# Kernel tuning notes

Measured on AMD Instinct MI355X. Metric: run time of the kernel, lower is better.

## Reference

```python
import jax, jax.numpy as jnp
import numpy as np
import math

DIM = 768
FFN_DIM = 4 * DIM
EPS = 1e-5

def layer_norm(x, gamma, beta):
    mu = jnp.mean(x, axis=-1, keepdims=True)
    var = jnp.var(x, axis=-1, keepdims=True)
    return (x - mu) * jax.lax.rsqrt(var + EPS) * gamma + beta

def setup_inputs() -> dict:
    key = jax.random.key(0)
    ks = jax.random.split(key, 8)
    b, n, d = 8, 2048, DIM
    s = 1.0 / math.sqrt(d)
    x = jax.random.normal(ks[0], (b, n, d), dtype=jnp.float32)
    Wq = jax.random.normal(ks[1], (d, d), dtype=jnp.float32) * s
    Wk = jax.random.normal(ks[2], (d, d), dtype=jnp.float32) * s
    Wv = jax.random.normal(ks[3], (d, d), dtype=jnp.float32) * s
    W1 = jax.random.normal(ks[4], (d, FFN_DIM), dtype=jnp.float32) * s
    b1 = jnp.zeros((FFN_DIM,), dtype=jnp.float32)
    W2 = jax.random.normal(ks[5], (FFN_DIM, d), dtype=jnp.float32) * (1.0 / math.sqrt(FFN_DIM))
    b2 = jnp.zeros((d,), dtype=jnp.float32)
    g1 = jnp.ones((d,), dtype=jnp.float32); be1 = jnp.zeros((d,), dtype=jnp.float32)
    g2 = jnp.ones((d,), dtype=jnp.float32); be2 = jnp.zeros((d,), dtype=jnp.float32)
    return {"x": x, "Wq": Wq, "Wk": Wk, "Wv": Wv, "ln1_g": g1, "ln1_b": be1,
            "W1": W1, "b1": b1, "W2": W2, "b2": b2, "ln2_g": g2, "ln2_b": be2}

def reference(x, Wq, Wk, Wv, ln1_g, ln1_b, W1, b1, W2, b2, ln2_g, ln2_b):
    # Self-attention (single head, full dim; dropout in eval mode => identity)
    Q = jnp.einsum('bnd,de->bne', x, Wq)
    K = jnp.einsum('bnd,de->bne', x, Wk)
    V = jnp.einsum('bnd,de->bne', x, Wv)
    scores = jnp.einsum('bnd,bmd->bnm', Q, K) / math.sqrt(DIM)  # [b,n,n]
    attn = jax.nn.softmax(scores, axis=-1)
    O = jnp.einsum('bnm,bmd->bnd', attn, V)
    h = layer_norm(x + O, ln1_g, ln1_b)
    # FFN with exact GELU (torch nn.GELU default)
    hidden = jax.nn.gelu(jnp.einsum('bnd,df->bnf', h, W1) + b1, approximate=False)
    out = jnp.einsum('bnf,fd->bnd', hidden, W2) + b2
    return layer_norm(h + out, ln2_g, ln2_b)
```

## Files before the change

### kernel.cpp

```cpp
#include <hip/hip_runtime.h>
#include <hip/hip_bf16.h>
#include <math.h>

using u16 = unsigned short;
typedef __bf16 bf16x8 __attribute__((ext_vector_type(8)));
typedef float f32x4 __attribute__((ext_vector_type(4)));
typedef u16 u16x8 __attribute__((ext_vector_type(8)));

__device__ __forceinline__ u16 f2b(float f) {
  union { float f; unsigned u; } c; c.f = f;
  unsigned r = c.u + 0x7fffu + ((c.u >> 16) & 1u);
  return (u16)(r >> 16);
}
__device__ __forceinline__ float b2f(u16 h) {
  union { unsigned u; float f; } c; c.u = ((unsigned)h) << 16;
  return c.f;
}

__device__ __forceinline__ float fast_gelu(float t) {
  float y = fminf(1.5957691216f * t + 0.07135481283f * t * t * t, 80.f);
  float e = __expf(y);
  return t * e * (1.0f / (e + 1.0f));
}

#define EPI_BF16 0
#define EPI_BF16_SCALE 1
#define EPI_GELU_BIAS 2
#define EPI_F32_BIAS 3

#define GLDS16(src, dst)                                                     \
  __builtin_amdgcn_global_load_lds(                                          \
      (const __attribute__((address_space(1))) void*)(src),                  \
      (__attribute__((address_space(3))) void*)(dst), 16, 0, 0)

__device__ __forceinline__ int xswz(int o, int n) {
  int q = n >> 3, r = n & 7, x = o & 7, i = o >> 3;
  return (x < r ? x * (q + 1) : r * (q + 1) + (x - r) * q) + i;
}

template <int EPI>
__device__ __forceinline__ void epi_store(
    void* Cg, const float* bias, float v, long long off, int ccol, float scale)
{
  if (EPI == EPI_BF16) {
    ((u16*)Cg)[off] = f2b(v);
  } else if (EPI == EPI_BF16_SCALE) {
    ((u16*)Cg)[off] = f2b(v * scale);
  } else if (EPI == EPI_GELU_BIAS) {
    ((u16*)Cg)[off] = f2b(fast_gelu(v + bias[ccol]));
  } else {
    ((float*)Cg)[off] = v + bias[ccol];
  }
}

template <int EPI>
__global__ __launch_bounds__(512, 2) void gemm256(
    const u16* __restrict__ Ag, const u16* __restrict__ Bg,
    void* __restrict__ Cg, const float* __restrict__ bias,
    int nbx, int K, float scale, int lda, int ldb, int ldc,
    long long sAz, long long sBz, long long sCz)
{
  __shared__ __align__(16) u16 lds[65536];

  const int tid = threadIdx.x;
  const int wave = tid >> 6, lane = tid & 63;
  const int wr = wave >> 2, wc = wave & 3;
  const int id = xswz(blockIdx.x, gridDim.x);
  const int bx = id % nbx, by = id / nbx;
  const int m0 = by * 256, n0 = bx * 256;
  const long long z = blockIdx.z;
  const u16* A = Ag + z * sAz + (long long)m0 * lda;
  const u16* B = Bg + z * sBz + (long long)n0 * ldb;

  const int rA = wave * 32 + (lane >> 2);
  const int slot = (lane & 3) ^ ((rA >> 1) & 3);
  const u16* a0 = A + (long long)rA * lda + slot * 8;
  const u16* a1 = a0 + (long long)16 * lda;
  const u16* b0 = B + (long long)rA * ldb + slot * 8;
  const u16* b1 = b0 + (long long)16 * ldb;
  const int d0 = wave * 32 * 32;
  const int d1 = (wave * 32 + 16) * 32;

  int offA[8], offB[4];
#pragma unroll
  for (int mf = 0; mf < 8; ++mf) {
    int r = wr * 128 + mf * 16 + (lane & 15);
    int b = r * 64 + ((lane >> 4) << 4);
    offA[mf] = b ^ (((b >> 7) & 3) << 4);
  }
#pragma unroll
  for (int nf = 0; nf < 4; ++nf) {
    int r = wc * 64 + nf * 16 + (lane & 15);
    int b = r * 64 + ((lane >> 4) << 4);
    offB[nf] = b ^ (((b >> 7) & 3) << 4);
  }

  f32x4 acc[8][4];
#pragma unroll
  for (int m = 0; m < 8; ++m)
#pragma unroll
    for (int n = 0; n < 4; ++n) acc[m][n] = f32x4{0.f, 0.f, 0.f, 0.f};

  const char* ldsc = (const char*)lds;
  const int NT = K >> 6;

  GLDS16(a0, lds + 0 * 8192 + d0);  GLDS16(a1, lds + 0 * 8192 + d1);
  GLDS16(b0, lds + 2 * 8192 + d0);  GLDS16(b1, lds + 2 * 8192 + d1);
  GLDS16(a0 + 32, lds + 1 * 8192 + d0);  GLDS16(a1 + 32, lds + 1 * 8192 + d1);
  GLDS16(b0 + 32, lds + 3 * 8192 + d0);  GLDS16(b1 + 32, lds + 3 * 8192 + d1);
  asm volatile("s_waitcnt vmcnt(4)" ::: "memory");
  asm volatile("s_barrier" ::: "memory");

  for (int t = 0; t < NT; ++t) {
    const int buf = t & 1, nb = buf ^ 1;
    const int kc = (t + 1 < NT) ? ((t + 1) << 6) : 0;
    const char* pA0 = ldsc + (buf * 4 + 0) * 16384;
    const char* pA1 = ldsc + (buf * 4 + 1) * 16384;
    const char* pB0 = ldsc + (buf * 4 + 2) * 16384;
    const char* pB1 = ldsc + (buf * 4 + 3) * 16384;
    u16* q = lds + nb * 4 * 8192;

    bf16x8 Af[4], Bf[4];

    GLDS16(a0 + kc, q + 0 * 8192 + d0);
    GLDS16(a1 + kc, q + 0 * 8192 + d1);
#pragma unroll
    for (int m = 0; m < 4; ++m) Af[m] = *(const bf16x8*)(pA0 + offA[m]);
#pragma unroll
    for (int n = 0; n < 4; ++n) Bf[n] = *(const bf16x8*)(pB0 + offB[n]);
    asm volatile("s_barrier" ::: "memory");
    __builtin_amdgcn_s_setprio(1);
#pragma unroll
    for (int m = 0; m < 4; ++m)
#pragma unroll
      for (int n = 0; n < 4; ++n)
        acc[m][n] = __builtin_amdgcn_mfma_f32_16x16x32_bf16(Af[m], Bf[n], acc[m][n], 0, 0, 0);
    __builtin_amdgcn_s_setprio(0);
    asm volatile("s_barrier" ::: "memory");

    GLDS16(b0 + kc, q + 2 * 8192 + d0);
    GLDS16(b1 + kc, q + 2 * 8192 + d1);
#pragma unroll
    for (int m = 0; m < 4; ++m) Af[m] = *(const bf16x8*)(pA0 + offA[4 + m]);
    asm volatile("s_barrier" ::: "memory");
    __builtin_amdgcn_s_setprio(1);
#pragma unroll
    for (int m = 0; m < 4; ++m)
#pragma unroll
      for (int n = 0; n < 4; ++n)
        acc[4 + m][n] = __builtin_amdgcn_mfma_f32_16x16x32_bf16(Af[m], Bf[n], acc[4 + m][n], 0, 0, 0);
    __builtin_amdgcn_s_setprio(0);
    asm volatile("s_waitcnt vmcnt(4)" ::: "memory");
    asm volatile("s_barrier" ::: "memory");

    GLDS16(a0 + kc + 32, q + 1 * 8192 + d0);
    GLDS16(a1 + kc + 32, q + 1 * 8192 + d1);
#pragma unroll
    for (int m = 0; m < 4; ++m) Af[m] = *(const bf16x8*)(pA1 + offA[m]);
#pragma unroll
    for (int n = 0; n < 4; ++n) Bf[n] = *(const bf16x8*)(pB1 + offB[n]);
    asm volatile("s_barrier" ::: "memory");
    __builtin_amdgcn_s_setprio(1);
#pragma unroll
    for (int m = 0; m < 4; ++m)
#pragma unroll
      for (int n = 0; n < 4; ++n)
        acc[m][n] = __builtin_amdgcn_mfma_f32_16x16x32_bf16(Af[m], Bf[n], acc[m][n], 0, 0, 0);
    __builtin_amdgcn_s_setprio(0);
    asm volatile("s_barrier" ::: "memory");

    GLDS16(b0 + kc + 32, q + 3 * 8192 + d0);
    GLDS16(b1 + kc + 32, q + 3 * 8192 + d1);
#pragma unroll
    for (int m = 0; m < 4; ++m) Af[m] = *(const bf16x8*)(pA1 + offA[4 + m]);
    asm volatile("s_barrier" ::: "memory");
    __builtin_amdgcn_s_setprio(1);
#pragma unroll
    for (int m = 0; m < 4; ++m)
#pragma unroll
      for (int n = 0; n < 4; ++n)
        acc[4 + m][n] = __builtin_amdgcn_mfma_f32_16x16x32_bf16(Af[m], Bf[n], acc[4 + m][n], 0, 0, 0);
    __builtin_amdgcn_s_setprio(0);
    asm volatile("s_waitcnt vmcnt(4)" ::: "memory");
    asm volatile("s_barrier" ::: "memory");
  }

#pragma unroll
  for (int mf = 0; mf < 8; ++mf) {
#pragma unroll
    for (int nf = 0; nf < 4; ++nf) {
      const int crow = m0 + wr * 128 + mf * 16 + (lane >> 4) * 4;
      const int ccol = n0 + wc * 64 + nf * 16 + (lane & 15);
#pragma unroll
      for (int j = 0; j < 4; ++j) {
        const long long off = (long long)(crow + j) * ldc + ccol + z * sCz;
        epi_store<EPI>(Cg, bias, acc[mf][nf][j], off, ccol, scale);
      }
    }
  }
}

template <int EPI>
__global__ __launch_bounds__(256, 2) void gemm128(
    const u16* __restrict__ Ag, const u16* __restrict__ Bg,
    void* __restrict__ Cg, const float* __restrict__ bias,
    int nbx, int K, float scale, int lda, int ldb, int ldc,
    long long sAz, long long sBz, long long sCz)
{
  __shared__ __align__(16) u16 lds[32768];

  const int tid = threadIdx.x;
  const int wave = tid >> 6, lane = tid & 63;
  const int wr = wave >> 1, wc = wave & 1;
  const int id = xswz(blockIdx.x, gridDim.x);
  const int bx = id % nbx, by = id / nbx;
  const int m0 = by * 128, n0 = bx * 128;
  const long long z = blockIdx.z;
  const u16* A = Ag + z * sAz + (long long)m0 * lda;
  const u16* B = Bg + z * sBz + (long long)n0 * ldb;

  const int rA = wave * 32 + (lane >> 2);
  const int slot = (lane & 3) ^ ((rA >> 1) & 3);
  const u16* a0 = A + (long long)rA * lda + slot * 8;
  const u16* a1 = a0 + (long long)16 * lda;
  const u16* b0 = B + (long long)rA * ldb + slot * 8;
  const u16* b1 = b0 + (long long)16 * ldb;
  const int d0 = wave * 32 * 32;
  const int d1 = (wave * 32 + 16) * 32;

  int offA[4], offB[4];
#pragma unroll
  for (int f = 0; f < 4; ++f) {
    int ra = wr * 64 + f * 16 + (lane & 15);
    int ba = ra * 64 + ((lane >> 4) << 4);
    offA[f] = ba ^ (((ba >> 7) & 3) << 4);
    int rb = wc * 64 + f * 16 + (lane & 15);
    int bb = rb * 64 + ((lane >> 4) << 4);
    offB[f] = bb ^ (((bb >> 7) & 3) << 4);
  }

  f32x4 acc[4][4];
#pragma unroll
  for (int m = 0; m < 4; ++m)
#pragma unroll
    for (int n = 0; n < 4; ++n) acc[m][n] = f32x4{0.f, 0.f, 0.f, 0.f};

  const char* ldsc = (const char*)lds;
  const int NT = K >> 6;

  GLDS16(a0, lds + 0 * 4096 + d0);  GLDS16(a1, lds + 0 * 4096 + d1);
  GLDS16(b0, lds + 2 * 4096 + d0);  GLDS16(b1, lds + 2 * 4096 + d1);
  GLDS16(a0 + 32, lds + 1 * 4096 + d0);  GLDS16(a1 + 32, lds + 1 * 4096 + d1);
  GLDS16(b0 + 32, lds + 3 * 4096 + d0);  GLDS16(b1 + 32, lds + 3 * 4096 + d1);
  asm volatile("s_waitcnt vmcnt(4)" ::: "memory");
  asm volatile("s_barrier" ::: "memory");

  for (int t = 0; t < NT; ++t) {
    const int buf = t & 1, nb = buf ^ 1;
    const int kc = (t + 1 < NT) ? ((t + 1) << 6) : 0;
    const char* pA0 = ldsc + (buf * 4 + 0) * 8192;
    const char* pA1 = ldsc + (buf * 4 + 1) * 8192;
    const char* pB0 = ldsc + (buf * 4 + 2) * 8192;
    const char* pB1 = ldsc + (buf * 4 + 3) * 8192;
    u16* q = lds + nb * 4 * 4096;

    bf16x8 Af[4], Bf[4];

    GLDS16(a0 + kc, q + 0 * 4096 + d0);  GLDS16(a1 + kc, q + 0 * 4096 + d1);
    GLDS16(b0 + kc, q + 2 * 4096 + d0);  GLDS16(b1 + kc, q + 2 * 4096 + d1);
#pragma unroll
    for (int m = 0; m < 4; ++m) Af[m] = *(const bf16x8*)(pA0 + offA[m]);
#pragma unroll
    for (int n = 0; n < 4; ++n) Bf[n] = *(const bf16x8*)(pB0 + offB[n]);
    asm volatile("s_barrier" ::: "memory");
    __builtin_amdgcn_s_setprio(1);
#pragma unroll
    for (int m = 0; m < 4; ++m)
#pragma unroll
      for (int n = 0; n < 4; ++n)
        acc[m][n] = __builtin_amdgcn_mfma_f32_16x16x32_bf16(Af[m], Bf[n], acc[m][n], 0, 0, 0);
    __builtin_amdgcn_s_setprio(0);
    asm volatile("s_waitcnt vmcnt(4)" ::: "memory");
    asm volatile("s_barrier" ::: "memory");

    GLDS16(a0 + kc + 32, q + 1 * 4096 + d0);  GLDS16(a1 + kc + 32, q + 1 * 4096 + d1);
    GLDS16(b0 + kc + 32, q + 3 * 4096 + d0);  GLDS16(b1 + kc + 32, q + 3 * 4096 + d1);
#pragma unroll
    for (int m = 0; m < 4; ++m) Af[m] = *(const bf16x8*)(pA1 + offA[m]);
#pragma unroll
    for (int n = 0; n < 4; ++n) Bf[n] = *(const bf16x8*)(pB1 + offB[n]);
    asm volatile("s_barrier" ::: "memory");
    __builtin_amdgcn_s_setprio(1);
#pragma unroll
    for (int m = 0; m < 4; ++m)
#pragma unroll
      for (int n = 0; n < 4; ++n)
        acc[m][n] = __builtin_amdgcn_mfma_f32_16x16x32_bf16(Af[m], Bf[n], acc[m][n], 0, 0, 0);
    __builtin_amdgcn_s_setprio(0);
    asm volatile("s_waitcnt vmcnt(4)" ::: "memory");
    asm volatile("s_barrier" ::: "memory");
  }

#pragma unroll
  for (int mf = 0; mf < 4; ++mf) {
#pragma unroll
    for (int nf = 0; nf < 4; ++nf) {
      const int crow = m0 + wr * 64 + mf * 16 + (lane >> 4) * 4;
      const int ccol = n0 + wc * 64 + nf * 16 + (lane & 15);
#pragma unroll
      for (int j = 0; j < 4; ++j) {
        const long long off = (long long)(crow + j) * ldc + ccol + z * sCz;
        epi_store<EPI>(Cg, bias, acc[mf][nf][j], off, ccol, scale);
      }
    }
  }
}

__global__ __launch_bounds__(256) void cast_f32_bf16(
    const float* __restrict__ x, u16* __restrict__ y, long long n4)
{
  const long long i = (long long)blockIdx.x * 256 + threadIdx.x;
  if (i >= n4) return;
  const float4 v = ((const float4*)x)[i];
  ushort4 o;
  o.x = f2b(v.x); o.y = f2b(v.y); o.z = f2b(v.z); o.w = f2b(v.w);
  ((ushort4*)y)[i] = o;
}

template <bool SRC_BF16>
__global__ __launch_bounds__(256) void transpose_cast(
    const void* __restrict__ srcv, u16* __restrict__ dst, int R, int C, int ldsrc,
    long long szSrc, long long szDst)
{
  __shared__ float tile[32][33];
  const long long zs = (long long)blockIdx.z * szSrc;
  const long long zd = (long long)blockIdx.z * szDst;
  const int c0 = blockIdx.x * 32, r0 = blockIdx.y * 32;
  const int tx = threadIdx.x & 31, ty = threadIdx.x >> 5;
#pragma unroll
  for (int i = 0; i < 4; ++i) {
    const int r = r0 + ty + i * 8;
    float v;
    if (SRC_BF16) v = b2f(((const u16*)srcv)[zs + (long long)r * ldsrc + c0 + tx]);
    else          v = ((const float*)srcv)[zs + (long long)r * ldsrc + c0 + tx];
    tile[ty + i * 8][tx] = v;
  }
  __syncthreads();
#pragma unroll
  for (int i = 0; i < 4; ++i) {
    const int c = c0 + ty + i * 8;
    dst[zd + (long long)c * R + r0 + tx] = f2b(tile[tx][ty + i * 8]);
  }
}

__global__ __launch_bounds__(256) void softmax_rows(
    u16* __restrict__ S, int ncol)
{
  __shared__ float red[8];
  const long long row = blockIdx.x;
  u16* s = S + row * ncol;
  const int t = threadIdx.x;

  const u16x8 u = *(const u16x8*)&s[t * 8];
  float v[8];
#pragma unroll
  for (int j = 0; j < 8; ++j) v[j] = b2f(u[j]);

  float mx = v[0];
#pragma unroll
  for (int j = 1; j < 8; ++j) mx = fmaxf(mx, v[j]);
  for (int o = 32; o; o >>= 1) mx = fmaxf(mx, __shfl_xor(mx, o));
  if ((t & 63) == 0) red[t >> 6] = mx;
  __syncthreads();
  mx = fmaxf(fmaxf(red[0], red[1]), fmaxf(red[2], red[3]));

  float sum = 0.f;
#pragma unroll
  for (int j = 0; j < 8; ++j) { v[j] = __expf(v[j] - mx); sum += v[j]; }
  for (int o = 32; o; o >>= 1) sum += __shfl_xor(sum, o);
  if ((t & 63) == 0) red[4 + (t >> 6)] = sum;
  __syncthreads();
  sum = red[4] + red[5] + red[6] + red[7];

  const float inv = 1.0f / sum;
  u16x8 o8;
#pragma unroll
  for (int j = 0; j < 8; ++j) o8[j] = f2b(v[j] * inv);
  *(u16x8*)&s[t * 8] = o8;
}

__global__ __launch_bounds__(256) void ln1_kernel(
    const float* __restrict__ x, const u16* __restrict__ O,
    const float* __restrict__ g, const float* __restrict__ be,
    u16* __restrict__ h)
{
  __shared__ float red[8];
  const long long row = blockIdx.x;
  const float* xr = x + row * 768;
  const u16* orow = O + row * 768;
  const int t = threadIdx.x, base = t * 3;

  float v[3];
#pragma unroll
  for (int j = 0; j < 3; ++j) v[j] = xr[base + j] + b2f(orow[base + j]);
  float s = v[0] + v[1] + v[2];
  float ss = v[0] * v[0] + v[1] * v[1] + v[2] * v[2];
  for (int o = 32; o; o >>= 1) { s += __shfl_xor(s, o); ss += __shfl_xor(ss, o); }
  if ((t & 63) == 0) { red[t >> 6] = s; red[4 + (t >> 6)] = ss; }
  __syncthreads();
  s = red[0] + red[1] + red[2] + red[3];
  ss = red[4] + red[5] + red[6] + red[7];
  const float mu = s * (1.0f / 768.0f);
  const float var = ss * (1.0f / 768.0f) - mu * mu;
  const float inv = rsqrtf(var + 1e-5f);
#pragma unroll
  for (int j = 0; j < 3; ++j) {
    const float o = (v[j] - mu) * inv * g[base + j] + be[base + j];
    h[row * 768 + base + j] = f2b(o);
  }
}

__global__ __launch_bounds__(256) void ln2_kernel(
    const u16* __restrict__ h, const float* __restrict__ oflt,
    const float* __restrict__ g, const float* __restrict__ be,
    float* __restrict__ y)
{
  __shared__ float red[8];
  const long long row = blockIdx.x;
  const u16* hr = h + row * 768;
  const float* orow = oflt + row * 768;
  const int t = threadIdx.x, base = t * 3;

  float v[3];
#pragma unroll
  for (int j = 0; j < 3; ++j) v[j] = b2f(hr[base + j]) + orow[base + j];
  float s = v[0] + v[1] + v[2];
  float ss = v[0] * v[0] + v[1] * v[1] + v[2] * v[2];
  for (int o = 32; o; o >>= 1) { s += __shfl_xor(s, o); ss += __shfl_xor(ss, o); }
  if ((t & 63) == 0) { red[t >> 6] = s; red[4 + (t >> 6)] = ss; }
  __syncthreads();
  s = red[0] + red[1] + red[2] + red[3];
  ss = red[4] + red[5] + red[6] + red[7];
  const float mu = s * (1.0f / 768.0f);
  const float var = ss * (1.0f / 768.0f) - mu * mu;
  const float inv = rsqrtf(var + 1e-5f);
#pragma unroll
  for (int j = 0; j < 3; ++j) {
    y[row * 768 + base + j] = (v[j] - mu) * inv * g[base + j] + be[base + j];
  }
}

extern "C" void kernel_launch(void* const* d_in, const int* in_sizes, int n_in,
                              void* d_out, int out_size, void* d_ws, size_t ws_size,
                              hipStream_t stream)
{
  const int Bb = 8, Nn = 2048, D = 768, F = 3072, E = 2304;
  const int M = Bb * Nn;
  const long long MD = (long long)M * D;

  const float* x   = (const float*)d_in[0];
  const float* Wq  = (const float*)d_in[1];
  const float* Wk  = (const float*)d_in[2];
  const float* Wv  = (const float*)d_in[3];
  const float* g1  = (const float*)d_in[4];
  const float* be1 = (const float*)d_in[5];
  const float* W1  = (const float*)d_in[6];
  const float* b1  = (const float*)d_in[7];
  const float* W2  = (const float*)d_in[8];
  const float* b2  = (const float*)d_in[9];
  const float* g2  = (const float*)d_in[10];
  const float* be2 = (const float*)d_in[11];

  u16* xb    = (u16*)d_out;
  u16* wqkvt = xb + MD;
  u16* wqt = wqkvt;
  u16* wkt = wqkvt + 768 * 768;
  u16* wvt = wqkvt + 2 * 768 * 768;

  char* w = (char*)d_ws;
  size_t off = 0;
  auto alloc = [&](size_t bytes) { void* p = w + off; off += bytes; return p; };
  u16* w1t = (u16*)alloc((size_t)F * D * 2);
  u16* w2t = (u16*)alloc((size_t)D * F * 2);
  u16* hb  = (u16*)alloc((size_t)MD * 2);
  u16* qkv = (u16*)alloc((size_t)M * E * 2);
  u16* Vt  = (u16*)alloc((size_t)Bb * D * Nn * 2);
  u16* S   = (u16*)alloc((size_t)Bb * Nn * Nn * 2);
  u16* O   = (u16*)alloc((size_t)MD * 2);
  u16*   hidden = qkv;
  float* outf   = (float*)S;

  const dim3 tcb(256);
  const float scl = 0.03608439182435161f;

  cast_f32_bf16<<<(unsigned)(MD / 4 / 256), 256, 0, stream>>>(x, xb, MD / 4);
  transpose_cast<false><<<dim3(D / 32, D / 32, 1), tcb, 0, stream>>>(Wq, wqt, D, D, D, 0, 0);
  transpose_cast<false><<<dim3(D / 32, D / 32, 1), tcb, 0, stream>>>(Wk, wkt, D, D, D, 0, 0);
  transpose_cast<false><<<dim3(D / 32, D / 32, 1), tcb, 0, stream>>>(Wv, wvt, D, D, D, 0, 0);
  transpose_cast<false><<<dim3(F / 32, D / 32, 1), tcb, 0, stream>>>(W1, w1t, D, F, F, 0, 0);
  transpose_cast<false><<<dim3(D / 32, F / 32, 1), tcb, 0, stream>>>(W2, w2t, F, D, D, 0, 0);

  gemm256<EPI_BF16><<<dim3(9 * 64, 1, 1), 512, 0, stream>>>(
      xb, wqkvt, qkv, nullptr, 9, D, 1.f, D, D, E, 0, 0, 0);

  transpose_cast<true><<<dim3(D / 32, Nn / 32, Bb), tcb, 0, stream>>>(
      qkv + 1536, Vt, Nn, D, E, (long long)Nn * E, (long long)D * Nn);

  gemm128<EPI_BF16_SCALE><<<dim3(16 * 16, 1, Bb), 256, 0, stream>>>(
      qkv, qkv + 768, S, nullptr, 16, D, scl, E, E, Nn,
      (long long)Nn * E, (long long)Nn * E, (long long)Nn * Nn);

  softmax_rows<<<M, 256, 0, stream>>>(S, Nn);

  gemm128<EPI_BF16><<<dim3(6 * 16, 1, Bb), 256, 0, stream>>>(
      S, Vt, O, nullptr, 6, Nn, 1.f, Nn, Nn, D,
      (long long)Nn * Nn, (long long)D * Nn, (long long)Nn * D);

  ln1_kernel<<<M, 256, 0, stream>>>(x, O, g1, be1, hb);

  gemm256<EPI_GELU_BIAS><<<dim3(12 * 64, 1, 1), 512, 0, stream>>>(
      hb, w1t, hidden, b1, 12, D, 1.f, D, D, F, 0, 0, 0);

  gemm128<EPI_F32_BIAS><<<dim3(6 * 128, 1, 1), 256, 0, stream>>>(
      hidden, w2t, outf, b2, 6, F, 1.f, F, F, D, 0, 0, 0);

  ln2_kernel<<<M, 256, 0, stream>>>(hb, outf, g2, be2, (float*)d_out);
}
```

Baseline: 520.4 us.

## Compute V transposed directly, use 256-tile QK^T, bf16 FFN output, fewer barriers

Several changes land together. V^T is now produced by a GEMM of Wv^T against x, which removes the separate V projection and its transpose pass. The QK^T scores GEMM moves to the 256-tile kernel, and the second FFN GEMM writes bf16 instead of fp32, roughly halving that write and the read in LN2. The 256 and 128 GEMM main loops also issue all prefetch loads earlier and drop most intra-iteration barriers; this risks LDS read/write races and adds bf16 rounding error on the FFN output.

```diff
diff --git a/kernel.cpp b/kernel.cpp
--- a/kernel.cpp
+++ b/kernel.cpp
@@ -27,6 +27,7 @@
 #define EPI_BF16_SCALE 1
 #define EPI_GELU_BIAS 2
 #define EPI_F32_BIAS 3
+#define EPI_BF16_BIAS 4
 
 #define GLDS16(src, dst)                                                     \
   __builtin_amdgcn_global_load_lds(                                          \
@@ -48,8 +49,10 @@
     ((u16*)Cg)[off] = f2b(v * scale);
   } else if (EPI == EPI_GELU_BIAS) {
     ((u16*)Cg)[off] = f2b(fast_gelu(v + bias[ccol]));
+  } else if (EPI == EPI_F32_BIAS) {
+    ((float*)Cg)[off] = v + bias[ccol];
   } else {
-    ((float*)Cg)[off] = v + bias[ccol];
+    ((u16*)Cg)[off] = f2b(v + bias[ccol]);
   }
 }
 
@@ -122,13 +125,12 @@
 
     bf16x8 Af[4], Bf[4];
 
-    GLDS16(a0 + kc, q + 0 * 8192 + d0);
-    GLDS16(a1 + kc, q + 0 * 8192 + d1);
+    GLDS16(a0 + kc, q + 0 * 8192 + d0);  GLDS16(a1 + kc, q + 0 * 8192 + d1);
+    GLDS16(b0 + kc, q + 2 * 8192 + d0);  GLDS16(b1 + kc, q + 2 * 8192 + d1);
 #pragma unroll
     for (int m = 0; m < 4; ++m) Af[m] = *(const bf16x8*)(pA0 + offA[m]);
 #pragma unroll
     for (int n = 0; n < 4; ++n) Bf[n] = *(const bf16x8*)(pB0 + offB[n]);
-    asm volatile("s_barrier" ::: "memory");
     __builtin_amdgcn_s_setprio(1);
 #pragma unroll
     for (int m = 0; m < 4; ++m)
@@ -136,13 +138,11 @@
       for (int n = 0; n < 4; ++n)
         acc[m][n] = __builtin_amdgcn_mfma_f32_16x16x32_bf16(Af[m], Bf[n], acc[m][n], 0, 0, 0);
     __builtin_amdgcn_s_setprio(0);
-    asm volatile("s_barrier" ::: "memory");
-
-    GLDS16(b0 + kc, q + 2 * 8192 + d0);
-    GLDS16(b1 + kc, q + 2 * 8192 + d1);
+
+    GLDS16(a0 + kc + 32, q + 1 * 8192 + d0);  GLDS16(a1 + kc + 32, q + 1 * 8192 + d1);
+    GLDS16(b0 + kc + 32, q + 3 * 8192 + d0);  GLDS16(b1 + kc + 32, q + 3 * 8192 + d1);
 #pragma unroll
     for (int m = 0; m < 4; ++m) Af[m] = *(const bf16x8*)(pA0 + offA[4 + m]);
-    asm volatile("s_barrier" ::: "memory");
     __builtin_amdgcn_s_setprio(1);
 #pragma unroll
     for (int m = 0; m < 4; ++m)
@@ -150,16 +150,13 @@
       for (int n = 0; n < 4; ++n)
         acc[4 + m][n] = __builtin_amdgcn_mfma_f32_16x16x32_bf16(Af[m], Bf[n], acc[4 + m][n], 0, 0, 0);
     __builtin_amdgcn_s_setprio(0);
-    asm volatile("s_waitcnt vmcnt(4)" ::: "memory");
+    asm volatile("s_waitcnt vmcnt(8)" ::: "memory");
     asm volatile("s_barrier" ::: "memory");
 
-    GLDS16(a0 + kc + 32, q + 1 * 8192 + d0);
-    GLDS16(a1 + kc + 32, q + 1 * 8192 + d1);
 #pragma unroll
     for (int m = 0; m < 4; ++m) Af[m] = *(const bf16x8*)(pA1 + offA[m]);
 #pragma unroll
     for (int n = 0; n < 4; ++n) Bf[n] = *(const bf16x8*)(pB1 + offB[n]);
-    asm volatile("s_barrier" ::: "memory");
     __builtin_amdgcn_s_setprio(1);
 #pragma unroll
     for (int m = 0; m < 4; ++m)
@@ -167,13 +164,9 @@
       for (int n = 0; n < 4; ++n)
         acc[m][n] = __builtin_amdgcn_mfma_f32_16x16x32_bf16(Af[m], Bf[n], acc[m][n], 0, 0, 0);
     __builtin_amdgcn_s_setprio(0);
-    asm volatile("s_barrier" ::: "memory");
-
-    GLDS16(b0 + kc + 32, q + 3 * 8192 + d0);
-    GLDS16(b1 + kc + 32, q + 3 * 8192 + d1);
+
 #pragma unroll
     for (int m = 0; m < 4; ++m) Af[m] = *(const bf16x8*)(pA1 + offA[4 + m]);
-    asm volatile("s_barrier" ::: "memory");
     __builtin_amdgcn_s_setprio(1);
 #pragma unroll
     for (int m = 0; m < 4; ++m)
@@ -272,7 +265,6 @@
     for (int m = 0; m < 4; ++m) Af[m] = *(const bf16x8*)(pA0 + offA[m]);
 #pragma unroll
     for (int n = 0; n < 4; ++n) Bf[n] = *(const bf16x8*)(pB0 + offB[n]);
-    asm volatile("s_barrier" ::: "memory");
     __builtin_amdgcn_s_setprio(1);
 #pragma unroll
     for (int m = 0; m < 4; ++m)
@@ -289,7 +281,6 @@
     for (int m = 0; m < 4; ++m) Af[m] = *(const bf16x8*)(pA1 + offA[m]);
 #pragma unroll
     for (int n = 0; n < 4; ++n) Bf[n] = *(const bf16x8*)(pB1 + offB[n]);
-    asm volatile("s_barrier" ::: "memory");
     __builtin_amdgcn_s_setprio(1);
 #pragma unroll
     for (int m = 0; m < 4; ++m)
@@ -421,19 +412,19 @@
 }
 
 __global__ __launch_bounds__(256) void ln2_kernel(
-    const u16* __restrict__ h, const float* __restrict__ oflt,
+    const u16* __restrict__ h, const u16* __restrict__ ob,
     const float* __restrict__ g, const float* __restrict__ be,
     float* __restrict__ y)
 {
   __shared__ float red[8];
   const long long row = blockIdx.x;
   const u16* hr = h + row * 768;
-  const float* orow = oflt + row * 768;
+  const u16* orow = ob + row * 768;
   const int t = threadIdx.x, base = t * 3;
 
   float v[3];
 #pragma unroll
-  for (int j = 0; j < 3; ++j) v[j] = b2f(hr[base + j]) + orow[base + j];
+  for (int j = 0; j < 3; ++j) v[j] = b2f(hr[base + j]) + b2f(orow[base + j]);
   float s = v[0] + v[1] + v[2];
   float ss = v[0] * v[0] + v[1] * v[1] + v[2] * v[2];
   for (int o = 32; o; o >>= 1) { s += __shfl_xor(s, o); ss += __shfl_xor(ss, o); }
@@ -454,7 +445,7 @@
                               void* d_out, int out_size, void* d_ws, size_t ws_size,
                               hipStream_t stream)
 {
-  const int Bb = 8, Nn = 2048, D = 768, F = 3072, E = 2304;
+  const int Bb = 8, Nn = 2048, D = 768, F = 3072, E = 1536;
   const int M = Bb * Nn;
   const long long MD = (long long)M * D;
 
@@ -471,11 +462,9 @@
   const float* g2  = (const float*)d_in[10];
   const float* be2 = (const float*)d_in[11];
 
-  u16* xb    = (u16*)d_out;
-  u16* wqkvt = xb + MD;
-  u16* wqt = wqkvt;
-  u16* wkt = wqkvt + 768 * 768;
-  u16* wvt = wqkvt + 2 * 768 * 768;
+  u16* xb   = (u16*)d_out;
+  u16* wqkt = xb + MD;
+  u16* wvt  = wqkt + (size_t)E * D;
 
   char* w = (char*)d_ws;
   size_t off = 0;
@@ -483,31 +472,32 @@
   u16* w1t = (u16*)alloc((size_t)F * D * 2);
   u16* w2t = (u16*)alloc((size_t)D * F * 2);
   u16* hb  = (u16*)alloc((size_t)MD * 2);
-  u16* qkv = (u16*)alloc((size_t)M * E * 2);
+  u16* qk  = (u16*)alloc((size_t)M * E * 2);
   u16* Vt  = (u16*)alloc((size_t)Bb * D * Nn * 2);
   u16* S   = (u16*)alloc((size_t)Bb * Nn * Nn * 2);
   u16* O   = (u16*)alloc((size_t)MD * 2);
-  u16*   hidden = qkv;
-  float* outf   = (float*)S;
+  u16* hidden = qk;
+  u16* outf   = qk + (size_t)M * F;
 
   const dim3 tcb(256);
   const float scl = 0.03608439182435161f;
 
   cast_f32_bf16<<<(unsigned)(MD / 4 / 256), 256, 0, stream>>>(x, xb, MD / 4);
-  transpose_cast<false><<<dim3(D / 32, D / 32, 1), tcb, 0, stream>>>(Wq, wqt, D, D, D, 0, 0);
-  transpose_cast<false><<<dim3(D / 32, D / 32, 1), tcb, 0, stream>>>(Wk, wkt, D, D, D, 0, 0);
+  transpose_cast<false><<<dim3(D / 32, D / 32, 1), tcb, 0, stream>>>(Wq, wqkt, D, D, D, 0, 0);
+  transpose_cast<false><<<dim3(D / 32, D / 32, 1), tcb, 0, stream>>>(Wk, wqkt + D * D, D, D, D, 0, 0);
   transpose_cast<false><<<dim3(D / 32, D / 32, 1), tcb, 0, stream>>>(Wv, wvt, D, D, D, 0, 0);
   transpose_cast<false><<<dim3(F / 32, D / 32, 1), tcb, 0, stream>>>(W1, w1t, D, F, F, 0, 0);
   transpose_cast<false><<<dim3(D / 32, F / 32, 1), tcb, 0, stream>>>(W2, w2t, F, D, D, 0, 0);
 
-  gemm256<EPI_BF16><<<dim3(9 * 64, 1, 1), 512, 0, stream>>>(
-      xb, wqkvt, qkv, nullptr, 9, D, 1.f, D, D, E, 0, 0, 0);
-
-  transpose_cast<true><<<dim3(D / 32, Nn / 32, Bb), tcb, 0, stream>>>(
-      qkv + 1536, Vt, Nn, D, E, (long long)Nn * E, (long long)D * Nn);
-
-  gemm128<EPI_BF16_SCALE><<<dim3(16 * 16, 1, Bb), 256, 0, stream>>>(
-      qkv, qkv + 768, S, nullptr, 16, D, scl, E, E, Nn,
+  gemm256<EPI_BF16><<<dim3(6 * 64, 1, 1), 512, 0, stream>>>(
+      xb, wqkt, qk, nullptr, 6, D, 1.f, D, D, E, 0, 0, 0);
+
+  gemm128<EPI_BF16><<<dim3(16 * 6, 1, Bb), 256, 0, stream>>>(
+      wvt, xb, Vt, nullptr, 16, D, 1.f, D, D, Nn,
+      0, (long long)Nn * D, (long long)D * Nn);
+
+  gemm256<EPI_BF16_SCALE><<<dim3(8 * 8, 1, Bb), 512, 0, stream>>>(
+      qk, qk + D, S, nullptr, 8, D, scl, E, E, Nn,
       (long long)Nn * E, (long long)Nn * E, (long long)Nn * Nn);
 
   softmax_rows<<<M, 256, 0, stream>>>(S, Nn);
@@ -521,7 +511,7 @@
   gemm256<EPI_GELU_BIAS><<<dim3(12 * 64, 1, 1), 512, 0, stream>>>(
       hb, w1t, hidden, b1, 12, D, 1.f, D, D, F, 0, 0, 0);
 
-  gemm128<EPI_F32_BIAS><<<dim3(6 * 128, 1, 1), 256, 0, stream>>>(
+  gemm128<EPI_BF16_BIAS><<<dim3(6 * 128, 1, 1), 256, 0, stream>>>(
       hidden, w2t, outf, b2, 6, F, 1.f, F, F, D, 0, 0, 0);
 
   ln2_kernel<<<M, 256, 0, stream>>>(hb, outf, g2, be2, (float*)d_out);
```

Result: faster. 501.1 us (-3.7%).
